# Optimization experiments

Hardware: AMD Instinct MI355X
Metric: run time of the kernel (lower is better)

## Reference

```python
import jax, jax.numpy as jnp
import numpy as np

B, S, I, W, H = 32, 2048, 32, 20, 128  # batch, seq_len, input_size, window_size, hidden_size
LN_EPS = 1e-5


def setup_inputs() -> dict:
    key = jax.random.key(0)
    ks = jax.random.split(key, 12)
    sc = lambda fan: 1.0 / np.sqrt(fan)
    x = jax.random.normal(ks[0], (B, S, I), jnp.float32)
    # encoder: Linear(W*I -> H) + LayerNorm(H) (+ GELU, dropout inactive at eval)
    W_enc = jax.random.normal(ks[1], (W * I, H), jnp.float32) * sc(W * I)
    b_enc = jnp.zeros((H,), jnp.float32)
    gamma = jnp.ones((H,), jnp.float32)
    beta = jnp.zeros((H,), jnp.float32)
    # comparator: Linear(2H->H), GELU, Linear(H->H//2), GELU, Linear(H//2->1), Sigmoid
    W1 = jax.random.normal(ks[2], (2 * H, H), jnp.float32) * sc(2 * H)
    b1 = jnp.zeros((H,), jnp.float32)
    W2 = jax.random.normal(ks[3], (H, H // 2), jnp.float32) * sc(H)
    b2 = jnp.zeros((H // 2,), jnp.float32)
    W3 = jax.random.normal(ks[4], (H // 2, 1), jnp.float32) * sc(H // 2)
    b3 = jnp.zeros((1,), jnp.float32)
    return dict(x=x, W_enc=W_enc, b_enc=b_enc, gamma=gamma, beta=beta,
                W1=W1, b1=b1, W2=W2, b2=b2, W3=W3, b3=b3)


def _gelu(v):
    return jax.nn.gelu(v, approximate=False)  # torch nn.GELU default is exact erf


def reference(x, W_enc, b_enc, gamma, beta, W1, b1, W2, b2, W3, b3):
    Bs, Ss, Is = x.shape
    Wd = W_enc.shape[0] // Is  # window_size
    nwin = Ss - Wd + 1
    # gather all sliding windows once: (B, nwin, Wd*I)
    idx = jnp.arange(nwin)[:, None] + jnp.arange(Wd)[None, :]
    win = x[:, idx, :].reshape(Bs, nwin, Wd * Is)
    # encoder: one big GEMM over all windows (before(t) == window at t-Wd, after(t) == window at t)
    h = win @ W_enc + b_enc
    mu = jnp.mean(h, axis=-1, keepdims=True)
    var = jnp.mean((h - mu) ** 2, axis=-1, keepdims=True)
    enc = _gelu((h - mu) / jnp.sqrt(var + LN_EPS) * gamma + beta)  # (B, nwin, H)
    T = Ss - 2 * Wd  # number of valid changepoint positions t in [Wd, Ss-Wd)
    combined = jnp.concatenate([enc[:, :T], enc[:, Wd:Wd + T]], axis=-1)  # (B, T, 2H)
    z = _gelu(combined @ W1 + b1)
    z = _gelu(z @ W2 + b2)
    p = jax.nn.sigmoid((z @ W3 + b3)[..., 0])  # (B, T)
    probs = jnp.pad(p, ((0, 0), (Wd, Wd)))  # zero pad to (B, S)
    return probs, probs > 0.5
```

## Files before the change

### kernel.cpp

```cpp
#include <hip/hip_runtime.h>
#include <hip/hip_bf16.h>
#include <math.h>

namespace {

constexpr int kB = 32;
constexpr int kS = 2048;
constexpr int kI = 32;
constexpr int kW = 20;
constexpr int kH = 128;
constexpr int kNwin = kS - kW + 1;
constexpr int kT = kS - 2 * kW;
constexpr float kEps = 1e-5f;
constexpr int FCAP = 16384;
constexpr float kMargin = 3e-3f;

typedef __attribute__((ext_vector_type(8))) _Float16 half8;
typedef __attribute__((ext_vector_type(8))) unsigned short ush8;
typedef __attribute__((ext_vector_type(4))) float f32x4;

#define GLD16(SRC, DST)                                                          \
    __builtin_amdgcn_global_load_lds(                                            \
        (const __attribute__((address_space(1))) unsigned*)(const void*)(SRC),   \
        (__attribute__((address_space(3))) unsigned*)(void*)(DST), 16, 0, 0)

__device__ __forceinline__ unsigned short f2h(float f) {
    _Float16 h = (_Float16)f;
    return __builtin_bit_cast(unsigned short, h);
}
__device__ __forceinline__ float gelu_exact(float v) {
    return 0.5f * v * (1.0f + erff(v * 0.70710678118654752440f));
}

constexpr size_t ENCB_OFF = 0;
constexpr size_t WEF_OFF  = 16777216;
constexpr size_t W1F_OFF  = WEF_OFF + 163840;
constexpr size_t W2F_OFF  = W1F_OFF + 65536;
constexpr size_t FC_OFF   = W2F_OFF + 16384;
constexpr size_t FL_OFF   = FC_OFF + 64;

__global__ void prep_kernel(const float* __restrict__ Wenc, const float* __restrict__ W1,
                            const float* __restrict__ W2,
                            unsigned short* __restrict__ WeF, unsigned short* __restrict__ W1F,
                            unsigned short* __restrict__ W2F)
{
    const int tid = blockIdx.x * blockDim.x + threadIdx.x;
    const int nth = gridDim.x * blockDim.x;
    for (int i = tid; i < 20 * 4 * 128 * 8; i += nth) {
        int j = i & 7, n = (i >> 3) & 127, rg = (i >> 10) & 3, kc = i >> 12;
        int k = kc * 32 + rg * 8 + j;
        WeF[i] = f2h(Wenc[(size_t)k * kH + n]);
    }
    for (int i = tid; i < 4 * 2 * 4 * 128 * 8; i += nth) {
        int j = i & 7, n = (i >> 3) & 127, rg = (i >> 10) & 3, ks = (i >> 12) & 1, kc = i >> 13;
        int k = kc * 64 + ks * 32 + rg * 8 + j;
        W1F[i] = f2h(W1[(size_t)k * kH + n]);
    }
    for (int i = tid; i < 2 * 2 * 4 * 64 * 8; i += nth) {
        int j = i & 7, n = (i >> 3) & 63, rg = (i >> 9) & 3, ks = (i >> 11) & 1, kc2 = i >> 12;
        int k = kc2 * 64 + ks * 32 + rg * 8 + j;
        W2F[i] = f2h(W2[(size_t)k * 64 + n]);
    }
}

constexpr int AP = 40;

__global__ __launch_bounds__(512, 4)
void enc_kernel(const float* __restrict__ x, const unsigned short* __restrict__ WeF,
                const float* __restrict__ benc, const float* __restrict__ gma,
                const float* __restrict__ bta, unsigned short* __restrict__ encb)
{
    __shared__ unsigned short xsh[147 * AP];
    __shared__ unsigned short wth[4096];
    __shared__ float red[2][128][2];

    const int tid = threadIdx.x, b = blockIdx.y, t0 = blockIdx.x * 128;
    const int l = tid & 63, w = tid >> 6;
    const int wr = w >> 1, wc = w & 1;
    const int cb = l & 15, rg = l >> 4;

    const float4* x4 = reinterpret_cast<const float4*>(x + (size_t)b * kS * kI);
    for (int i = tid; i < 147 * 8; i += 512) {
        int r = i >> 3, q = i & 7;
        int gr = t0 + r; if (gr > kS - 1) gr = kS - 1;
        float4 v = x4[gr * 8 + q];
        unsigned short h0 = f2h(v.x), h1 = f2h(v.y), h2 = f2h(v.z), h3 = f2h(v.w);
        *reinterpret_cast<uint2*>(&xsh[r * AP + q * 4]) =
            make_uint2((unsigned)h0 | ((unsigned)h1 << 16), (unsigned)h2 | ((unsigned)h3 << 16));
    }

    f32x4 acc[2][4];
    #pragma unroll
    for (int mi = 0; mi < 2; ++mi)
        #pragma unroll
        for (int nf = 0; nf < 4; ++nf) acc[mi][nf] = f32x4{0.f, 0.f, 0.f, 0.f};

    for (int kc = 0; kc < 20; ++kc) {
        __syncthreads();
        GLD16(WeF + (size_t)kc * 4096 + w * 512 + l * 8, &wth[w * 512]);
        __syncthreads();
        const int a0o = (wr * 32 + cb + kc) * AP + rg * 8;
        half8 a0 = *reinterpret_cast<const half8*>(&xsh[a0o]);
        half8 a1 = *reinterpret_cast<const half8*>(&xsh[a0o + 16 * AP]);
        #pragma unroll
        for (int nf = 0; nf < 4; ++nf) {
            const int bo = rg * 1024 + (wc * 64 + nf * 16 + cb) * 8;
            half8 bh = *reinterpret_cast<const half8*>(&wth[bo]);
            acc[0][nf] = __builtin_amdgcn_mfma_f32_16x16x32_f16(a0, bh, acc[0][nf], 0, 0, 0);
            acc[1][nf] = __builtin_amdgcn_mfma_f32_16x16x32_f16(a1, bh, acc[1][nf], 0, 0, 0);
        }
    }

    float bv[4], gv[4], btv[4];
    #pragma unroll
    for (int nf = 0; nf < 4; ++nf) {
        const int col = wc * 64 + nf * 16 + cb;
        bv[nf] = benc[col]; gv[nf] = gma[col]; btv[nf] = bta[col];
    }
    float h[2][4][4];
    #pragma unroll
    for (int mi = 0; mi < 2; ++mi)
        #pragma unroll
        for (int r = 0; r < 4; ++r) {
            float s = 0.f;
            #pragma unroll
            for (int nf = 0; nf < 4; ++nf) {
                h[mi][r][nf] = acc[mi][nf][r] + bv[nf];
                s += h[mi][r][nf];
            }
            s += __shfl_xor(s, 1); s += __shfl_xor(s, 2);
            s += __shfl_xor(s, 4); s += __shfl_xor(s, 8);
            if (cb == 0) red[0][wr * 32 + mi * 16 + rg * 4 + r][wc] = s;
        }
    __syncthreads();
    #pragma unroll
    for (int mi = 0; mi < 2; ++mi)
        #pragma unroll
        for (int r = 0; r < 4; ++r) {
            const int rl = wr * 32 + mi * 16 + rg * 4 + r;
            const float mu = (red[0][rl][0] + red[0][rl][1]) * (1.f / 128.f);
            float s2 = 0.f;
            #pragma unroll
            for (int nf = 0; nf < 4; ++nf) {
                h[mi][r][nf] -= mu;
                s2 += h[mi][r][nf] * h[mi][r][nf];
            }
            s2 += __shfl_xor(s2, 1); s2 += __shfl_xor(s2, 2);
            s2 += __shfl_xor(s2, 4); s2 += __shfl_xor(s2, 8);
            if (cb == 0) red[1][rl][wc] = s2;
        }
    __syncthreads();
    #pragma unroll
    for (int mi = 0; mi < 2; ++mi)
        #pragma unroll
        for (int r = 0; r < 4; ++r) {
            const int rl = wr * 32 + mi * 16 + rg * 4 + r;
            const int t = t0 + rl;
            const float var = (red[1][rl][0] + red[1][rl][1]) * (1.f / 128.f);
            const float rstd = 1.f / sqrtf(var + kEps);
            if (t < kNwin) {
                unsigned short* dst = encb + ((size_t)(b * kS + t)) * kH;
                #pragma unroll
                for (int nf = 0; nf < 4; ++nf) {
                    float v = gelu_exact(h[mi][r][nf] * rstd * gv[nf] + btv[nf]);
                    dst[wc * 64 + nf * 16 + cb] = f2h(v);
                }
            }
        }
}

constexpr int EPP = 72;

__global__ __launch_bounds__(512, 4)
void cmp_kernel(const unsigned short* __restrict__ encb,
                const unsigned short* __restrict__ W1F, const float* __restrict__ b1,
                const unsigned short* __restrict__ W2F, const float* __restrict__ b2,
                const float* __restrict__ W3, const float* __restrict__ b3,
                float* __restrict__ out, int* __restrict__ fcnt, unsigned* __restrict__ flist)
{
    __shared__ __align__(16) unsigned short pool[12800];
    __shared__ float prm[192];

    unsigned short* esh  = pool;
    unsigned short* wt1h = pool + 4608;

    const int tid = threadIdx.x, b = blockIdx.y, t0 = blockIdx.x * 64;
    const int l = tid & 63, w = tid >> 6;
    const int wr = w >> 1, wc = w & 1;
    const int cb = l & 15, rg = l >> 4;

    if (tid < 128) prm[tid] = b1[tid];
    else if (tid < 192) prm[tid] = b2[tid - 128];

    f32x4 acc1[4];
    #pragma unroll
    for (int nf = 0; nf < 4; ++nf) acc1[nf] = f32x4{0.f, 0.f, 0.f, 0.f};

    for (int kc = 0; kc < 4; ++kc) {
        const int ro = (kc < 2) ? 0 : kW, co = (kc & 1) * 64;
        __syncthreads();
        GLD16(W1F + (size_t)kc * 8192 + w * 512 + l * 8, &wt1h[w * 512]);
        GLD16(W1F + (size_t)kc * 8192 + 4096 + w * 512 + l * 8, &wt1h[4096 + w * 512]);
        {
            const int r = tid >> 3, qq = tid & 7;
            int gr = t0 + ro + r; if (gr > kNwin - 1) gr = kNwin - 1;
            *reinterpret_cast<ush8*>(&esh[r * EPP + qq * 8]) =
                *reinterpret_cast<const ush8*>(encb + ((size_t)(b * kS + gr)) * kH + co + qq * 8);
        }
        __syncthreads();
        #pragma unroll
        for (int ks = 0; ks < 2; ++ks) {
            const int ao = (wr * 16 + cb) * EPP + ks * 32 + rg * 8;
            half8 ah = *reinterpret_cast<const half8*>(&esh[ao]);
            #pragma unroll
            for (int nf = 0; nf < 4; ++nf) {
                const int bo = (ks * 4 + rg) * 1024 + (wc * 64 + nf * 16 + cb) * 8;
                half8 bh = *reinterpret_cast<const half8*>(&wt1h[bo]);
                acc1[nf] = __builtin_amdgcn_mfma_f32_16x16x32_f16(ah, bh, acc1[nf], 0, 0, 0);
            }
        }
    }
    __syncthreads();
    unsigned short* z1h = pool;
    unsigned short* w2h = pool + 8704;
    #pragma unroll
    for (int r = 0; r < 4; ++r) {
        const int row = wr * 16 + rg * 4 + r;
        #pragma unroll
        for (int nf = 0; nf < 4; ++nf) {
            const int col = wc * 64 + nf * 16 + cb;
            z1h[row * 136 + col] = f2h(gelu_exact(acc1[nf][r] + prm[col]));
        }
    }

    f32x4 acc2[2];
    #pragma unroll
    for (int nf = 0; nf < 2; ++nf) acc2[nf] = f32x4{0.f, 0.f, 0.f, 0.f};

    for (int kc2 = 0; kc2 < 2; ++kc2) {
        __syncthreads();
        GLD16(W2F + (size_t)kc2 * 4096 + w * 512 + l * 8, &w2h[w * 512]);
        __syncthreads();
        #pragma unroll
        for (int ks = 0; ks < 2; ++ks) {
            const int ao = (wr * 16 + cb) * 136 + kc2 * 64 + ks * 32 + rg * 8;
            half8 ah = *reinterpret_cast<const half8*>(&z1h[ao]);
            #pragma unroll
            for (int nf = 0; nf < 2; ++nf) {
                const int bo = (ks * 4 + rg) * 512 + (wc * 32 + nf * 16 + cb) * 8;
                half8 bh = *reinterpret_cast<const half8*>(&w2h[bo]);
                acc2[nf] = __builtin_amdgcn_mfma_f32_16x16x32_f16(ah, bh, acc2[nf], 0, 0, 0);
            }
        }
    }
    __syncthreads();
    float* z2f = reinterpret_cast<float*>(pool);
    #pragma unroll
    for (int r = 0; r < 4; ++r) {
        const int row = wr * 16 + rg * 4 + r;
        #pragma unroll
        for (int nf = 0; nf < 2; ++nf) {
            const int col = wc * 32 + nf * 16 + cb;
            z2f[row * 68 + col] = gelu_exact(acc2[nf][r] + prm[128 + col]);
        }
    }
    __syncthreads();

    if (tid < 64) {
        const int t = t0 + tid;
        if (t < kT) {
            float s = 0.f;
            #pragma unroll 8
            for (int k = 0; k < 64; ++k) s = fmaf(z2f[tid * 68 + k], W3[k], s);
            const float p = 1.f / (1.f + expf(-(s + b3[0])));
            out[(size_t)b * kS + t + kW] = p;
            out[(size_t)kB * kS + (size_t)b * kS + t + kW] = (p > 0.5f) ? 1.f : 0.f;
            if (fabsf(p - 0.5f) < kMargin) {
                int idx = atomicAdd(fcnt, 1);
                if (idx < FCAP) flist[idx] = ((unsigned)b << 16) | (unsigned)t;
            }
        }
    }
}

__global__ __launch_bounds__(256, 2)
void fix3_kernel(const float* __restrict__ x, const float* __restrict__ Wenc,
                 const float* __restrict__ benc, const float* __restrict__ gma,
                 const float* __restrict__ bta, const float* __restrict__ W1,
                 const float* __restrict__ b1, const float* __restrict__ W2,
                 const float* __restrict__ b2, const float* __restrict__ W3,
                 const float* __restrict__ b3, const int* __restrict__ fcnt,
                 const unsigned* __restrict__ flist, float* __restrict__ out)
{
    __shared__ float xw[1280 * 8];
    __shared__ float es[8][256];
    __shared__ float z1s[8][128];
    __shared__ float z2s[8][64];
    __shared__ float wredA[4][8];
    __shared__ float wredB[4][8];
    __shared__ unsigned pbt[8];

    const int tid = threadIdx.x;
    int n = *fcnt; if (n > FCAP) n = FCAP;
    const int nb = (n + 7) >> 3;

    for (int ib = blockIdx.x; ib < nb; ib += gridDim.x) {
        __syncthreads();
        if (tid < 8) {
            int idx = ib * 8 + tid; if (idx > n - 1) idx = n - 1;
            pbt[tid] = flist[idx];
        }
        __syncthreads();
        #pragma unroll
        for (int p = 0; p < 8; ++p) {
            const unsigned e = pbt[p];
            const int bb = (int)(e >> 16), tt = (int)(e & 0xFFFF);
            const float4* src = reinterpret_cast<const float4*>(
                x + ((size_t)bb * kS + tt) * kI);
            for (int j4 = tid; j4 < 320; j4 += 256) {
                float4 v = src[j4];
                float* dst = &xw[(j4 * 4) * 8 + p];
                dst[0] = v.x; dst[8] = v.y; dst[16] = v.z; dst[24] = v.w;
            }
        }
        __syncthreads();

        const int r = tid >> 7, c = tid & 127;
        const int wv = tid >> 6;
        float acc[8];
        #pragma unroll
        for (int p = 0; p < 8; ++p) acc[p] = 0.f;
        {
            const float* wp = Wenc + c;
            const int jb = r * 640;
            #pragma unroll 8
            for (int k = 0; k < 640; ++k) {
                const float wvv = wp[(size_t)k * kH];
                const float4 lo = *reinterpret_cast<const float4*>(&xw[(jb + k) * 8]);
                const float4 hi = *reinterpret_cast<const float4*>(&xw[(jb + k) * 8 + 4]);
                acc[0] = fmaf(lo.x, wvv, acc[0]);
                acc[1] = fmaf(lo.y, wvv, acc[1]);
                acc[2] = fmaf(lo.z, wvv, acc[2]);
                acc[3] = fmaf(lo.w, wvv, acc[3]);
                acc[4] = fmaf(hi.x, wvv, acc[4]);
                acc[5] = fmaf(hi.y, wvv, acc[5]);
                acc[6] = fmaf(hi.z, wvv, acc[6]);
                acc[7] = fmaf(hi.w, wvv, acc[7]);
            }
        }
        const float bc = benc[c];
        float hv[8];
        #pragma unroll
        for (int p = 0; p < 8; ++p) {
            hv[p] = acc[p] + bc;
            float s = hv[p];
            #pragma unroll
            for (int m = 1; m < 64; m <<= 1) s += __shfl_xor(s, m, 64);
            if ((tid & 63) == 0) wredA[wv][p] = s;
        }
        __syncthreads();
        #pragma unroll
        for (int p = 0; p < 8; ++p) {
            const float mu = (wredA[r * 2][p] + wredA[r * 2 + 1][p]) * (1.f / 128.f);
            hv[p] -= mu;
            float s2 = hv[p] * hv[p];
            #pragma unroll
            for (int m = 1; m < 64; m <<= 1) s2 += __shfl_xor(s2, m, 64);
            if ((tid & 63) == 0) wredB[wv][p] = s2;
        }
        __syncthreads();
        {
            const float gc = gma[c], btc = bta[c];
            #pragma unroll
            for (int p = 0; p < 8; ++p) {
                const float var = (wredB[r * 2][p] + wredB[r * 2 + 1][p]) * (1.f / 128.f);
                es[p][r * 128 + c] = gelu_exact(hv[p] * (1.f / sqrtf(var + kEps)) * gc + btc);
            }
        }
        __syncthreads();
        {
            const int ph = tid >> 7, j = tid & 127;
            float z[4] = {0.f, 0.f, 0.f, 0.f};
            #pragma unroll 4
            for (int k = 0; k < 256; ++k) {
                const float w1v = W1[(size_t)k * kH + j];
                #pragma unroll
                for (int pp = 0; pp < 4; ++pp)
                    z[pp] = fmaf(es[ph * 4 + pp][k], w1v, z[pp]);
            }
            const float b1j = b1[j];
            #pragma unroll
            for (int pp = 0; pp < 4; ++pp)
                z1s[ph * 4 + pp][j] = gelu_exact(z[pp] + b1j);
        }
        __syncthreads();
        {
            const int ph2 = tid >> 6, j = tid & 63;
            float z[2] = {0.f, 0.f};
            #pragma unroll 4
            for (int k = 0; k < 128; ++k) {
                const float w2v = W2[(size_t)k * 64 + j];
                #pragma unroll
                for (int pp = 0; pp < 2; ++pp)
                    z[pp] = fmaf(z1s[ph2 * 2 + pp][k], w2v, z[pp]);
            }
            const float b2j = b2[j];
            #pragma unroll
            for (int pp = 0; pp < 2; ++pp)
                z2s[ph2 * 2 + pp][j] = gelu_exact(z[pp] + b2j);
        }
        __syncthreads();
        {
            const int p = tid >> 5, q = tid & 31;
            float s = z2s[p][q] * W3[q] + z2s[p][q + 32] * W3[q + 32];
            s += __shfl_xor(s, 1); s += __shfl_xor(s, 2); s += __shfl_xor(s, 4);
            s += __shfl_xor(s, 8); s += __shfl_xor(s, 16);
            if (q == 0) {
                const unsigned e = pbt[p];
                const int bb = (int)(e >> 16), tt = (int)(e & 0xFFFF);
                const float pr = 1.f / (1.f + expf(-(s + b3[0])));
                out[(size_t)bb * kS + tt + kW] = pr;
                out[(size_t)kB * kS + (size_t)bb * kS + tt + kW] = (pr > 0.5f) ? 1.f : 0.f;
            }
        }
    }
}

}

extern "C" void kernel_launch(void* const* d_in, const int* in_sizes, int n_in,
                              void* d_out, int out_size, void* d_ws, size_t ws_size,
                              hipStream_t stream)
{
    const float* x    = (const float*)d_in[0];
    const float* Wenc = (const float*)d_in[1];
    const float* benc = (const float*)d_in[2];
    const float* gma  = (const float*)d_in[3];
    const float* bta  = (const float*)d_in[4];
    const float* W1   = (const float*)d_in[5];
    const float* b1   = (const float*)d_in[6];
    const float* W2   = (const float*)d_in[7];
    const float* b2   = (const float*)d_in[8];
    const float* W3   = (const float*)d_in[9];
    const float* b3   = (const float*)d_in[10];
    float* out = (float*)d_out;

    char* ws = (char*)d_ws;
    unsigned short* encb  = (unsigned short*)(ws + ENCB_OFF);
    unsigned short* WeF   = (unsigned short*)(ws + WEF_OFF);
    unsigned short* W1F   = (unsigned short*)(ws + W1F_OFF);
    unsigned short* W2F   = (unsigned short*)(ws + W2F_OFF);
    int* fcnt             = (int*)(ws + FC_OFF);
    unsigned* flist       = (unsigned*)(ws + FL_OFF);

    hipMemsetAsync(d_out, 0, (size_t)out_size * sizeof(float), stream);
    hipMemsetAsync(fcnt, 0, 64, stream);

    prep_kernel<<<256, 256, 0, stream>>>(Wenc, W1, W2, WeF, W1F, W2F);
    enc_kernel<<<dim3(16, kB), 512, 0, stream>>>(x, WeF, benc, gma, bta, encb);
    cmp_kernel<<<dim3(32, kB), 512, 0, stream>>>(encb, W1F, b1, W2F, b2, W3, b3,
                                                 out, fcnt, flist);
    fix3_kernel<<<1024, 256, 0, stream>>>(x, Wenc, benc, gma, bta, W1, b1, W2, b2, W3, b3,
                                          fcnt, flist, out);
}
```

Measured before the change: 135.9 us.

## Stage weight chunks in LDS for fp32 fixup kernel and register-tile outputs

The fp32 recompute kernel for near-threshold positions now streams Wenc, W1 and W2 in 32 KB chunks into shared memory with async global-to-LDS loads, instead of reading weights per thread from global memory. Each thread computes a 2x4 or 1x4 register tile, and the LayerNorm reductions now stay within a 32-lane group using shuffles only. The grid is halved and the kernel exits early when there are no flagged positions. This is meant to cut global-memory weight traffic and barriers in the fixup pass, at the cost of more chunk-level syncs and higher LDS use per block.

```diff
diff --git a/kernel.cpp b/kernel.cpp
--- a/kernel.cpp
+++ b/kernel.cpp
@@ -284,7 +284,7 @@
 }
 
 __global__ __launch_bounds__(256, 2)
-void fix3_kernel(const float* __restrict__ x, const float* __restrict__ Wenc,
+void fix4_kernel(const float* __restrict__ x, const float* __restrict__ Wenc,
                  const float* __restrict__ benc, const float* __restrict__ gma,
                  const float* __restrict__ bta, const float* __restrict__ W1,
                  const float* __restrict__ b1, const float* __restrict__ W2,
@@ -292,16 +292,18 @@
                  const float* __restrict__ b3, const int* __restrict__ fcnt,
                  const unsigned* __restrict__ flist, float* __restrict__ out)
 {
-    __shared__ float xw[1280 * 8];
-    __shared__ float es[8][256];
-    __shared__ float z1s[8][128];
-    __shared__ float z2s[8][64];
-    __shared__ float wredA[4][8];
-    __shared__ float wredB[4][8];
+    __shared__ float Wc[8192];
+    __shared__ float xwc[1024];
+    __shared__ float es[2048];
+    __shared__ float z1s[1024];
+    __shared__ float z2s[512];
     __shared__ unsigned pbt[8];
 
     const int tid = threadIdx.x;
+    const int wv = tid >> 6, l = tid & 63;
+    const int p = tid >> 5, cq = tid & 31;
     int n = *fcnt; if (n > FCAP) n = FCAP;
+    if (n <= 0) return;
     const int nb = (n + 7) >> 3;
 
     for (int ib = blockIdx.x; ib < nb; ib += gridDim.x) {
@@ -311,111 +313,128 @@
             pbt[tid] = flist[idx];
         }
         __syncthreads();
-        #pragma unroll
-        for (int p = 0; p < 8; ++p) {
-            const unsigned e = pbt[p];
-            const int bb = (int)(e >> 16), tt = (int)(e & 0xFFFF);
-            const float4* src = reinterpret_cast<const float4*>(
-                x + ((size_t)bb * kS + tt) * kI);
-            for (int j4 = tid; j4 < 320; j4 += 256) {
-                float4 v = src[j4];
-                float* dst = &xw[(j4 * 4) * 8 + p];
-                dst[0] = v.x; dst[8] = v.y; dst[16] = v.z; dst[24] = v.w;
-            }
-        }
-        __syncthreads();
-
-        const int r = tid >> 7, c = tid & 127;
-        const int wv = tid >> 6;
-        float acc[8];
-        #pragma unroll
-        for (int p = 0; p < 8; ++p) acc[p] = 0.f;
+
+        float acc[2][4];
+        #pragma unroll
+        for (int r = 0; r < 2; ++r)
+            #pragma unroll
+            for (int j = 0; j < 4; ++j) acc[r][j] = 0.f;
+
+        for (int kc = 0; kc < 10; ++kc) {
+            __syncthreads();
+            {
+                const float* src = Wenc + (size_t)kc * 8192;
+                #pragma unroll
+                for (int q = 0; q < 8; ++q)
+                    GLD16(src + (wv * 8 + q) * 256 + l * 4, &Wc[(wv * 8 + q) * 256]);
+            }
+            {
+                const int kq = tid & 15, pp = (tid >> 4) & 7, r = tid >> 7;
+                const unsigned e = pbt[pp];
+                const int bb = (int)(e >> 16), tt = (int)(e & 0xFFFF);
+                const float4 v = *reinterpret_cast<const float4*>(
+                    x + ((size_t)bb * kS + tt + r * kW) * kI + kc * 64 + kq * 4);
+                *reinterpret_cast<float4*>(&xwc[(r * 8 + pp) * 64 + kq * 4]) = v;
+            }
+            __syncthreads();
+            #pragma unroll 4
+            for (int kk = 0; kk < 64; ++kk) {
+                const float a0 = xwc[p * 64 + kk];
+                const float a1 = xwc[(8 + p) * 64 + kk];
+                const float4 wv4 = *reinterpret_cast<const float4*>(&Wc[kk * 128 + cq * 4]);
+                acc[0][0] = fmaf(a0, wv4.x, acc[0][0]);
+                acc[0][1] = fmaf(a0, wv4.y, acc[0][1]);
+                acc[0][2] = fmaf(a0, wv4.z, acc[0][2]);
+                acc[0][3] = fmaf(a0, wv4.w, acc[0][3]);
+                acc[1][0] = fmaf(a1, wv4.x, acc[1][0]);
+                acc[1][1] = fmaf(a1, wv4.y, acc[1][1]);
+                acc[1][2] = fmaf(a1, wv4.z, acc[1][2]);
+                acc[1][3] = fmaf(a1, wv4.w, acc[1][3]);
+            }
+        }
+
+        const float4 bv = *reinterpret_cast<const float4*>(benc + cq * 4);
+        const float4 gv = *reinterpret_cast<const float4*>(gma + cq * 4);
+        const float4 bt = *reinterpret_cast<const float4*>(bta + cq * 4);
+        #pragma unroll
+        for (int r = 0; r < 2; ++r) {
+            float hv[4];
+            hv[0] = acc[r][0] + bv.x; hv[1] = acc[r][1] + bv.y;
+            hv[2] = acc[r][2] + bv.z; hv[3] = acc[r][3] + bv.w;
+            float s = hv[0] + hv[1] + hv[2] + hv[3];
+            s += __shfl_xor(s, 1); s += __shfl_xor(s, 2); s += __shfl_xor(s, 4);
+            s += __shfl_xor(s, 8); s += __shfl_xor(s, 16);
+            const float mu = s * (1.f / 128.f);
+            float s2 = 0.f;
+            #pragma unroll
+            for (int j = 0; j < 4; ++j) { hv[j] -= mu; s2 += hv[j] * hv[j]; }
+            s2 += __shfl_xor(s2, 1); s2 += __shfl_xor(s2, 2); s2 += __shfl_xor(s2, 4);
+            s2 += __shfl_xor(s2, 8); s2 += __shfl_xor(s2, 16);
+            const float rstd = 1.f / sqrtf(s2 * (1.f / 128.f) + kEps);
+            float o[4];
+            o[0] = gelu_exact(hv[0] * rstd * gv.x + bt.x);
+            o[1] = gelu_exact(hv[1] * rstd * gv.y + bt.y);
+            o[2] = gelu_exact(hv[2] * rstd * gv.z + bt.z);
+            o[3] = gelu_exact(hv[3] * rstd * gv.w + bt.w);
+            *reinterpret_cast<float4*>(&es[p * 256 + r * 128 + cq * 4]) =
+                make_float4(o[0], o[1], o[2], o[3]);
+        }
+
         {
-            const float* wp = Wenc + c;
-            const int jb = r * 640;
-            #pragma unroll 8
-            for (int k = 0; k < 640; ++k) {
-                const float wvv = wp[(size_t)k * kH];
-                const float4 lo = *reinterpret_cast<const float4*>(&xw[(jb + k) * 8]);
-                const float4 hi = *reinterpret_cast<const float4*>(&xw[(jb + k) * 8 + 4]);
-                acc[0] = fmaf(lo.x, wvv, acc[0]);
-                acc[1] = fmaf(lo.y, wvv, acc[1]);
-                acc[2] = fmaf(lo.z, wvv, acc[2]);
-                acc[3] = fmaf(lo.w, wvv, acc[3]);
-                acc[4] = fmaf(hi.x, wvv, acc[4]);
-                acc[5] = fmaf(hi.y, wvv, acc[5]);
-                acc[6] = fmaf(hi.z, wvv, acc[6]);
-                acc[7] = fmaf(hi.w, wvv, acc[7]);
-            }
-        }
-        const float bc = benc[c];
-        float hv[8];
-        #pragma unroll
-        for (int p = 0; p < 8; ++p) {
-            hv[p] = acc[p] + bc;
-            float s = hv[p];
-            #pragma unroll
-            for (int m = 1; m < 64; m <<= 1) s += __shfl_xor(s, m, 64);
-            if ((tid & 63) == 0) wredA[wv][p] = s;
-        }
-        __syncthreads();
-        #pragma unroll
-        for (int p = 0; p < 8; ++p) {
-            const float mu = (wredA[r * 2][p] + wredA[r * 2 + 1][p]) * (1.f / 128.f);
-            hv[p] -= mu;
-            float s2 = hv[p] * hv[p];
-            #pragma unroll
-            for (int m = 1; m < 64; m <<= 1) s2 += __shfl_xor(s2, m, 64);
-            if ((tid & 63) == 0) wredB[wv][p] = s2;
-        }
+            float z[4] = {0.f, 0.f, 0.f, 0.f};
+            for (int kc1 = 0; kc1 < 4; ++kc1) {
+                __syncthreads();
+                const float* src = W1 + (size_t)kc1 * 8192;
+                #pragma unroll
+                for (int q = 0; q < 8; ++q)
+                    GLD16(src + (wv * 8 + q) * 256 + l * 4, &Wc[(wv * 8 + q) * 256]);
+                __syncthreads();
+                #pragma unroll 4
+                for (int kk = 0; kk < 64; ++kk) {
+                    const float a = es[p * 256 + kc1 * 64 + kk];
+                    const float4 wv4 = *reinterpret_cast<const float4*>(&Wc[kk * 128 + cq * 4]);
+                    z[0] = fmaf(a, wv4.x, z[0]);
+                    z[1] = fmaf(a, wv4.y, z[1]);
+                    z[2] = fmaf(a, wv4.z, z[2]);
+                    z[3] = fmaf(a, wv4.w, z[3]);
+                }
+            }
+            const float4 b1v = *reinterpret_cast<const float4*>(b1 + cq * 4);
+            *reinterpret_cast<float4*>(&z1s[p * 128 + cq * 4]) = make_float4(
+                gelu_exact(z[0] + b1v.x), gelu_exact(z[1] + b1v.y),
+                gelu_exact(z[2] + b1v.z), gelu_exact(z[3] + b1v.w));
+        }
+
         __syncthreads();
         {
-            const float gc = gma[c], btc = bta[c];
-            #pragma unroll
-            for (int p = 0; p < 8; ++p) {
-                const float var = (wredB[r * 2][p] + wredB[r * 2 + 1][p]) * (1.f / 128.f);
-                es[p][r * 128 + c] = gelu_exact(hv[p] * (1.f / sqrtf(var + kEps)) * gc + btc);
-            }
-        }
-        __syncthreads();
-        {
-            const int ph = tid >> 7, j = tid & 127;
+            #pragma unroll
+            for (int q = 0; q < 8; ++q)
+                GLD16(W2 + (wv * 8 + q) * 256 + l * 4, &Wc[(wv * 8 + q) * 256]);
+        }
+        __syncthreads();
+        if (cq < 16) {
             float z[4] = {0.f, 0.f, 0.f, 0.f};
             #pragma unroll 4
-            for (int k = 0; k < 256; ++k) {
-                const float w1v = W1[(size_t)k * kH + j];
-                #pragma unroll
-                for (int pp = 0; pp < 4; ++pp)
-                    z[pp] = fmaf(es[ph * 4 + pp][k], w1v, z[pp]);
-            }
-            const float b1j = b1[j];
-            #pragma unroll
-            for (int pp = 0; pp < 4; ++pp)
-                z1s[ph * 4 + pp][j] = gelu_exact(z[pp] + b1j);
-        }
-        __syncthreads();
+            for (int kk = 0; kk < 128; ++kk) {
+                const float a = z1s[p * 128 + kk];
+                const float4 wv4 = *reinterpret_cast<const float4*>(&Wc[kk * 64 + cq * 4]);
+                z[0] = fmaf(a, wv4.x, z[0]);
+                z[1] = fmaf(a, wv4.y, z[1]);
+                z[2] = fmaf(a, wv4.z, z[2]);
+                z[3] = fmaf(a, wv4.w, z[3]);
+            }
+            const float4 b2v = *reinterpret_cast<const float4*>(b2 + cq * 4);
+            *reinterpret_cast<float4*>(&z2s[p * 64 + cq * 4]) = make_float4(
+                gelu_exact(z[0] + b2v.x), gelu_exact(z[1] + b2v.y),
+                gelu_exact(z[2] + b2v.z), gelu_exact(z[3] + b2v.w));
+        }
+        __syncthreads();
+
         {
-            const int ph2 = tid >> 6, j = tid & 63;
-            float z[2] = {0.f, 0.f};
-            #pragma unroll 4
-            for (int k = 0; k < 128; ++k) {
-                const float w2v = W2[(size_t)k * 64 + j];
-                #pragma unroll
-                for (int pp = 0; pp < 2; ++pp)
-                    z[pp] = fmaf(z1s[ph2 * 2 + pp][k], w2v, z[pp]);
-            }
-            const float b2j = b2[j];
-            #pragma unroll
-            for (int pp = 0; pp < 2; ++pp)
-                z2s[ph2 * 2 + pp][j] = gelu_exact(z[pp] + b2j);
-        }
-        __syncthreads();
-        {
-            const int p = tid >> 5, q = tid & 31;
-            float s = z2s[p][q] * W3[q] + z2s[p][q + 32] * W3[q + 32];
+            float s = z2s[p * 64 + cq] * W3[cq] + z2s[p * 64 + cq + 32] * W3[cq + 32];
             s += __shfl_xor(s, 1); s += __shfl_xor(s, 2); s += __shfl_xor(s, 4);
             s += __shfl_xor(s, 8); s += __shfl_xor(s, 16);
-            if (q == 0) {
+            if (cq == 0) {
                 const unsigned e = pbt[p];
                 const int bb = (int)(e >> 16), tt = (int)(e & 0xFFFF);
                 const float pr = 1.f / (1.f + expf(-(s + b3[0])));
@@ -460,6 +479,6 @@
     enc_kernel<<<dim3(16, kB), 512, 0, stream>>>(x, WeF, benc, gma, bta, encb);
     cmp_kernel<<<dim3(32, kB), 512, 0, stream>>>(encb, W1F, b1, W2F, b2, W3, b3,
                                                  out, fcnt, flist);
-    fix3_kernel<<<1024, 256, 0, stream>>>(x, Wenc, benc, gma, bta, W1, b1, W2, b2, W3, b3,
-                                          fcnt, flist, out);
-}
+    fix4_kernel<<<512, 256, 0, stream>>>(x, Wenc, benc, gma, bta, W1, b1, W2, b2, W3, b3,
+                                         fcnt, flist, out);
+}
```

After: 112.6 us. 17.1% less time.
